# Performance work log

Hardware: AMD Instinct MI355X
Metric: run time of the kernel (lower is better)

## Reference

```python
import jax, jax.numpy as jnp
import numpy as np

E, H = 256, 4
DH = E // H                      # head dim 64
DHALF, N, R, K = 256, 16, 16, 5  # mamba d_inner//2, d_state, dt_rank, d_conv
B, L = 2, 2048


def _ln(x, g, b):
    m = jnp.mean(x, -1, keepdims=True)
    v = jnp.var(x, -1, keepdims=True)
    return (x - m) * jax.lax.rsqrt(v + 1e-5) * g + b


def _rotate_half(x):
    y = x.reshape(x.shape[:-1] + (-1, 2))
    return jnp.stack((-y[..., 1], y[..., 0]), -1).reshape(x.shape)


def _dwconv(x, w):  # x: (B,C,L), w: (C,1,K), depthwise 'same' conv, no bias (conv_bias//2 == 0)
    return jax.lax.conv_general_dilated(
        x, w, (1,), 'SAME', feature_group_count=x.shape[1],
        dimension_numbers=('NCH', 'OIH', 'NCH'))


def _selective_scan(x, dt, A_log, Bm, Cm, Dp, dt_bias):
    # x, dt: (B,Dh,L); Bm, Cm: (B,N,L); A_log: (Dh,N); Dp, dt_bias: (Dh,)
    A = -jnp.exp(A_log)
    delta = jax.nn.softplus(dt + dt_bias[None, :, None])
    seq = (jnp.moveaxis(delta, 2, 0), jnp.moveaxis(x, 2, 0),
           jnp.moveaxis(Bm, 2, 0), jnp.moveaxis(Cm, 2, 0))
    h0 = jnp.zeros((x.shape[0], A.shape[0], A.shape[1]), x.dtype)

    def step(h, inp):
        d_l, x_l, B_l, C_l = inp
        h = jnp.exp(d_l[:, :, None] * A) * h + (d_l * x_l)[:, :, None] * B_l[:, None, :]
        return h, jnp.einsum('bdn,bn->bd', h, C_l)

    _, ys = jax.lax.scan(step, h0, seq)
    return jnp.moveaxis(ys, 0, 2) + Dp[None, :, None] * x


def _forward(desc0, desc1, pe0, pe1, qkv_w, qkv_b, attn_out_w, attn_out_b,
             ma_ffn_w1, ma_ffn_b1, ma_ffn_g, ma_ffn_beta, ma_ffn_w2, ma_ffn_b2,
             m_in_w, m_convx_w, m_convz_w, m_xproj_w, m_dt_w, m_dt_b, m_Alog, m_D, m_out_w,
             ca_qk_w, ca_qk_b, ca_v_w, ca_v_b, ca_out_w, ca_out_b,
             ca_ffn_w1, ca_ffn_b1, ca_ffn_g, ca_ffn_beta, ca_ffn_w2, ca_ffn_b2):

    def mamba_twopath(x_in):
        xz = jnp.swapaxes(x_in @ m_in_w.T, 1, 2)           # (B, 2*Dh, L)
        xc, zc = xz[:, :DHALF], xz[:, DHALF:]
        xc = jax.nn.silu(_dwconv(xc, m_convx_w))
        zc = jax.nn.silu(_dwconv(zc, m_convz_w))
        x_dbl = jnp.einsum('bdl,kd->bkl', xc, m_xproj_w)   # (B, R+2N, L)
        # dt_proj applies its bias here AND the same bias is re-added inside the scan
        # (delta_bias), exactly as in the torch source.
        dt = jnp.einsum('brl,dr->bdl', x_dbl[:, :R], m_dt_w) + m_dt_b[None, :, None]
        Bm, Cm = x_dbl[:, R:R + N], x_dbl[:, R + N:]
        y = _selective_scan(xc, dt, m_Alog, Bm, Cm, m_D, m_dt_b)  # (B, Dh, L)
        return jnp.swapaxes(y, 1, 2) @ m_out_w.T, jnp.swapaxes(zc, 1, 2) @ m_out_w.T

    def ma_ffn(h):
        h = _ln(h @ ma_ffn_w1.T + ma_ffn_b1, ma_ffn_g, ma_ffn_beta)
        return jax.nn.gelu(h, approximate=False) @ ma_ffn_w2.T + ma_ffn_b2

    def mamba_attention(x, pe):
        b, l, _ = x.shape
        qkv = (x @ qkv_w.T + qkv_b).reshape(b, l, H, DH, 3)
        qkv = jnp.swapaxes(qkv, 1, 2)                       # (B,H,L,DH,3)
        q, k, v = qkv[..., 0], qkv[..., 1], qkv[..., 2]
        q = q * pe[0] + _rotate_half(q) * pe[1]
        k = k * pe[0] + _rotate_half(k) * pe[1]
        attn = jax.nn.softmax(jnp.einsum('bhid,bhjd->bhij', q, k) * DH ** -0.5, -1)
        o = jnp.einsum('bhij,bhjd->bhid', attn, v)
        o = jnp.swapaxes(o, 1, 2).reshape(b, l, E) @ attn_out_w.T + attn_out_b
        s_x, c_x = mamba_twopath(x)
        return x + ma_ffn(jnp.concatenate([x, o, s_x, c_x], -1))

    def ca_ffn(h):
        h = _ln(h @ ca_ffn_w1.T + ca_ffn_b1, ca_ffn_g, ca_ffn_beta)
        return jax.nn.gelu(h, approximate=False) @ ca_ffn_w2.T + ca_ffn_b2

    def split_heads(t):
        b, l, _ = t.shape
        return jnp.swapaxes(t.reshape(b, l, H, DH), 1, 2)

    def cross_attn(x0, x1):
        s = DH ** -0.25  # scale**0.5 applied to both qk0 and qk1
        qk0 = split_heads(x0 @ ca_qk_w.T + ca_qk_b) * s
        qk1 = split_heads(x1 @ ca_qk_w.T + ca_qk_b) * s
        v0 = split_heads(x0 @ ca_v_w.T + ca_v_b)
        v1 = split_heads(x1 @ ca_v_w.T + ca_v_b)
        sim = jnp.einsum('bhid,bhjd->bhij', qk0, qk1)       # (B,H,L0,L1)
        m0 = jnp.einsum('bhij,bhjd->bhid', jax.nn.softmax(sim, -1), v1)
        m1 = jnp.einsum('bhji,bhjd->bhid', jax.nn.softmax(sim, -2), v0)
        b, l = x0.shape[0], x0.shape[1]
        m0 = jnp.swapaxes(m0, 1, 2).reshape(b, l, E) @ ca_out_w.T + ca_out_b
        m1 = jnp.swapaxes(m1, 1, 2).reshape(b, x1.shape[1], E) @ ca_out_w.T + ca_out_b
        x0 = x0 + ca_ffn(jnp.concatenate([x0, m0], -1))
        x1 = x1 + ca_ffn(jnp.concatenate([x1, m1], -1))
        return x0, x1

    d0 = mamba_attention(desc0, pe0)
    d1 = mamba_attention(desc1, pe1)
    return cross_attn(d0, d1)


def setup_inputs():
    key = jax.random.key(0)
    ks = jax.random.split(key, 32)
    rn = lambda i, shape, s=0.02: jax.random.normal(ks[i], shape, jnp.float32) * s
    rng = np.random.default_rng(0)
    dt = np.exp(rng.uniform(size=DHALF) * (np.log(0.1) - np.log(0.001)) + np.log(0.001))
    inv_dt = dt + np.log(-np.expm1(-dt))
    return {
        'desc0': jax.random.normal(ks[0], (B, L, E), jnp.float32),
        'desc1': jax.random.normal(ks[1], (B, L, E), jnp.float32),
        'pe0': jax.random.normal(ks[2], (2, B, 1, L, DH), jnp.float32),
        'pe1': jax.random.normal(ks[3], (2, B, 1, L, DH), jnp.float32),
        'qkv_w': rn(4, (3 * E, E)), 'qkv_b': rn(5, (3 * E,)),
        'attn_out_w': rn(6, (E, E)), 'attn_out_b': rn(7, (E,)),
        'ma_ffn_w1': rn(8, (2 * E, 4 * E)), 'ma_ffn_b1': rn(9, (2 * E,)),
        'ma_ffn_g': jnp.ones((2 * E,), jnp.float32), 'ma_ffn_beta': jnp.zeros((2 * E,), jnp.float32),
        'ma_ffn_w2': rn(10, (E, 2 * E)), 'ma_ffn_b2': rn(11, (E,)),
        'm_in_w': rn(12, (2 * DHALF, E)),
        'm_convx_w': rn(13, (DHALF, 1, K), 0.2), 'm_convz_w': rn(14, (DHALF, 1, K), 0.2),
        'm_xproj_w': rn(15, (R + 2 * N, DHALF)),
        'm_dt_w': rn(16, (DHALF, R), R ** -0.5),
        'm_dt_b': jnp.asarray(inv_dt, jnp.float32),
        'm_Alog': jnp.log(jnp.broadcast_to(jnp.arange(1, N + 1, dtype=jnp.float32), (DHALF, N))),
        'm_D': jnp.ones((DHALF,), jnp.float32),
        'm_out_w': rn(17, (E, DHALF)),
        'ca_qk_w': rn(18, (E, E)), 'ca_qk_b': rn(19, (E,)),
        'ca_v_w': rn(20, (E, E)), 'ca_v_b': rn(21, (E,)),
        'ca_out_w': rn(22, (E, E)), 'ca_out_b': rn(23, (E,)),
        'ca_ffn_w1': rn(24, (2 * E, 2 * E)), 'ca_ffn_b1': rn(25, (2 * E,)),
        'ca_ffn_g': jnp.ones((2 * E,), jnp.float32), 'ca_ffn_beta': jnp.zeros((2 * E,), jnp.float32),
        'ca_ffn_w2': rn(26, (E, 2 * E)), 'ca_ffn_b2': rn(27, (E,)),
    }


def reference(desc0, desc1, pe0, pe1, qkv_w, qkv_b, attn_out_w, attn_out_b,
              ma_ffn_w1, ma_ffn_b1, ma_ffn_g, ma_ffn_beta, ma_ffn_w2, ma_ffn_b2,
              m_in_w, m_convx_w, m_convz_w, m_xproj_w, m_dt_w, m_dt_b, m_Alog, m_D, m_out_w,
              ca_qk_w, ca_qk_b, ca_v_w, ca_v_b, ca_out_w, ca_out_b,
              ca_ffn_w1, ca_ffn_b1, ca_ffn_g, ca_ffn_beta, ca_ffn_w2, ca_ffn_b2):
    return _forward(desc0, desc1, pe0, pe1, qkv_w, qkv_b, attn_out_w, attn_out_b,
                    ma_ffn_w1, ma_ffn_b1, ma_ffn_g, ma_ffn_beta, ma_ffn_w2, ma_ffn_b2,
                    m_in_w, m_convx_w, m_convz_w, m_xproj_w, m_dt_w, m_dt_b, m_Alog, m_D, m_out_w,
                    ca_qk_w, ca_qk_b, ca_v_w, ca_v_b, ca_out_w, ca_out_b,
                    ca_ffn_w1, ca_ffn_b1, ca_ffn_g, ca_ffn_beta, ca_ffn_w2, ca_ffn_b2)
```

## Files before the change

### kernel.cpp

```cpp
#include <hip/hip_runtime.h>

typedef unsigned short u16;
typedef short s16;
typedef s16 s16x8 __attribute__((ext_vector_type(8)));
typedef float f32x4 __attribute__((ext_vector_type(4)));

__device__ __forceinline__ float bf2f(u16 u){
  union { unsigned int i; float f; } v; v.i = ((unsigned int)u) << 16; return v.f;
}
__device__ __forceinline__ u16 f2bf(float f){
  union { float f; unsigned int u; } v; v.f = f;
  unsigned int r = (v.u + 0x7fffu + ((v.u >> 16) & 1u)) >> 16;
  return (u16)r;
}
__device__ __forceinline__ unsigned int cvtpk(float lo, float hi){
  unsigned int d;
  asm("v_cvt_pk_bf16_f32 %0, %1, %2" : "=v"(d) : "v"(lo), "v"(hi));
  return d;
}
__device__ __forceinline__ uint4 pack8(float4 a0, float4 a1){
  uint4 v;
  v.x = cvtpk(a0.x, a0.y); v.y = cvtpk(a0.z, a0.w);
  v.z = cvtpk(a1.x, a1.y); v.w = cvtpk(a1.z, a1.w);
  return v;
// ... 16 lines not shown
__device__ __forceinline__ float dppf(float x){
  return __int_as_float(__builtin_amdgcn_update_dpp(0, __float_as_int(x), C, 0xf, 0xf, true));
}
__device__ __forceinline__ float dppmax16(float v){
  v = fmaxf(v, dppf<0xB1>(v));
  v = fmaxf(v, dppf<0x4E>(v));
  v = fmaxf(v, dppf<0x141>(v));
  v = fmaxf(v, dppf<0x140>(v));
  return v;
}
__device__ __forceinline__ float dppsum16(float v){
  v += dppf<0xB1>(v);
  v += dppf<0x4E>(v);
  v += dppf<0x141>(v);
  v += dppf<0x140>(v);
  return v;
}

__global__ __launch_bounds__(256) void k_sniff(const unsigned int* __restrict__ w,
                                               int n, int* __restrict__ flag){
  __shared__ int cnt[256];
  int c = 0;
  for (int i = threadIdx.x; i < n; i += 256){
    unsigned e = (w[i] >> 7) & 0xFFu;
    c += (e >= 120u && e <= 127u) ? 1 : 0;
  }
  cnt[threadIdx.x] = c; __syncthreads();
  for (int s = 128; s > 0; s >>= 1){
    if (threadIdx.x < s) cnt[threadIdx.x] += cnt[threadIdx.x + s];
    __syncthreads();
  }
  if (threadIdx.x == 0) flag[0] = (2 * cnt[0] > n) ? 1 : 0;
  if (threadIdx.x == 1) flag[1] = 0;
}

struct WC { const void* src[11]; int off[12]; };
__global__ __launch_bounds__(256) void k_wconv(WC wc, u16* __restrict__ dst,
                                               const int* __restrict__ flagp){
  int fl = *flagp;
  int i = blockIdx.x * 256 + threadIdx.x;
  if (i >= wc.off[11]) return;
  int s = 0;
  #pragma unroll
  for (int t = 1; t < 11; ++t) s += (i >= wc.off[t]) ? 1 : 0;
  dst[i] = f2bf(ldw(wc.src[s], i - wc.off[s], fl));
}

__global__ __launch_bounds__(256) void k_pad(
  const void* __restrict__ wx, const void* __restrict__ wd,
  const void* __restrict__ bd,
  u16* __restrict__ px, u16* __restrict__ pd, float* __restrict__ pb,
  const int* __restrict__ flagp)
{
  int fl = *flagp;
  int i = blockIdx.x * 256 + threadIdx.x;
  if (i < 16384){
    int r = i >> 8, c = i & 255;
    px[i] = f2bf((r < 48) ? ldw(wx, r*256 + c, fl) : 0.f);
  } else if (i < 32768){
    int j = i - 16384;
    int n = j >> 6, k = j & 63;
    pd[j] = f2bf((k < 16) ? ldw(wd, n*16 + k, fl) : 0.f);
  } else if (i < 33024){
    pb[i - 32768] = ldw(bd, i - 32768, fl);
  }
}

__global__ __launch_bounds__(256) void k_gemm_mfma(
  const void* __restrict__ A0, int aflidx, int lda, int K, int N,
  const u16* __restrict__ W, const u16* __restrict__ W2, int nsplit, int wflidx,
  const void* __restrict__ bias,
  float* __restrict__ Cf0, u16* __restrict__ Cb, int ldc,
  float* __restrict__ C20, int ldc2,
  const void* __restrict__ resid, int rflidx, int ldr,
  const void* __restrict__ csrc, int cflidx, float* __restrict__ cdst,
  float oscale, int act_gelu, int outmode,
  const void* __restrict__ A1, long coff1, long c2off1,
  const int* __restrict__ flagp)
{
  const int fl  = flagp[0];
  const int afl = flagp[aflidx];
  const int wfl = flagp[wflidx];
  const int rfl = flagp[rflidx];
  const int cfl = flagp[cflidx];
  const void* A = A0;
  float* Cf = Cf0;
  float* C2 = C20;
  if (blockIdx.z){ A = A1; Cf += coff1; C2 += c2off1; }
  __shared__ u16 As[64*72];
  __shared__ u16 Bs[64*72];
  const int tid = threadIdx.x;
  const int w = tid >> 6, lane = tid & 63, quad = lane >> 4, m = lane & 15;
  const int m0 = blockIdx.y << 6, n0 = blockIdx.x << 6;
  const int srow = tid >> 2, sc0 = (tid & 3) << 4;
  const int reg2 = (n0 >= nsplit);
  const u16* Wp = reg2 ? W2 : W;
  const int nbase = reg2 ? nsplit : 0;

  f32x4 acc[4];
  #pragma unroll
  for (int ct = 0; ct < 4; ++ct) acc[ct] = (f32x4){0.f,0.f,0.f,0.f};

  for (int k0 = 0; k0 < K; k0 += 64){
    {
      long ab = (long)(m0 + srow) * lda + k0 + sc0;
      if (afl && !act_gelu){
        #pragma unroll
        for (int g = 0; g < 2; ++g)
          *(uint4*)&As[srow*72 + sc0 + g*8] = *(const uint4*)((const u16*)A + ab + g*8);
      } else {
        #pragma unroll
        for (int g = 0; g < 2; ++g){
          float4 a0 = ldw4(A, ab + g*8, afl);
          float4 a1 = ldw4(A, ab + g*8 + 4, afl);
          if (act_gelu){
            a0.x=gelu_f(a0.x); a0.y=gelu_f(a0.y); a0.z=gelu_f(a0.z); a0.w=gelu_f(a0.w);
            a1.x=gelu_f(a1.x); a1.y=gelu_f(a1.y); a1.z=gelu_f(a1.z); a1.w=gelu_f(a1.w);
// ... 35 lines not shown
      for (int r = 0; r < 4; ++r){
        float dl = acc[ct][r] + bv + bv;
        float delta = (dl > 20.f) ? dl : __logf(1.f + __expf(dl));
        dl4[r] = delta;
        dx4[r] = delta * ldw(resid, (long)(gmb + r) * ldr + gn, rfl);
      }
      *(float4*)&Cf[(long)gn * ldc + gmb] = make_float4(dl4[0], dl4[1], dl4[2], dl4[3]);
      *(float4*)&C2[(long)gn * ldc2 + gmb] = make_float4(dx4[0], dx4[1], dx4[2], dx4[3]);
    }
    return;
  }

  #pragma unroll
  for (int r = 0; r < 4; ++r){
    int gm = m0 + w*16 + quad*4 + r;
    #pragma unroll
    for (int ct = 0; ct < 4; ++ct){
      int gn = n0 + ct*16 + m;
      float v = acc[ct][r];
      if (reg2){
        C2[(long)gm * ldc2 + (gn - nsplit)] = v;
      } else {
        if (bias) v += ldw(bias, gn, wfl);
        v *= oscale;
        if (resid) v += ldw(resid, (long)gm * ldr + gn, rfl);
        long off = (long)gm * ldc + gn;
        if (outmode == 2){
          if (fl) Cb[off] = f2bf(v); else Cf[off] = v;
        } else if (outmode == 3){
          Cb[off] = f2bf(v);
        } else {
          Cf[off] = v;
        }
        if (cdst) cdst[(long)gm * ldc + gn] = ldw(csrc, (long)gm * 256 + gn, cfl);
      }
    }
  }
}

struct GB8 {
  const float* A[8]; const u16* W[8]; const void* bias[8];
  float* Cf[8]; u16* Cb[8]; const void* resid[8];
  const void* csrc[8]; float* cdst[8]; float osc[8];
  int cfl[8]; int wkoff[8]; int rfli[8];
  const float* aux[8]; const void* dvec;
};

__global__ __launch_bounds__(256) void k_gemmb(
  GB8 gb, int lda, int K, int N, int ldc, int ldr, int ldwq,
  int act_gelu, int outmode, const int* __restrict__ flagp)
{
  const int fl = flagp[0];
  const int z = blockIdx.z;
  const float* A = gb.A[z]; const u16* W = gb.W[z]; const void* bias = gb.bias[z];
  float* Cf = gb.Cf[z]; u16* Cb = gb.Cb[z]; const void* resid = gb.resid[z];
  const void* csrc = gb.csrc[z]; float* cdst = gb.cdst[z];
  const float osc = gb.osc[z];
  const int cfl = flagp[gb.cfl[z]];
  const int rfl = flagp[gb.rfli[z]];
  const int wkoff = gb.wkoff[z];
  const float* aux = gb.aux[z];

  __shared__ u16 As[64*72];
  __shared__ u16 Bs[64*72];
  const int tid = threadIdx.x;
  const int w = tid >> 6, lane = tid & 63, quad = lane >> 4, m = lane & 15;
  const int m0 = blockIdx.y << 6, n0 = blockIdx.x << 6;
  const int srow = tid >> 2, sc0 = (tid & 3) << 4;

  f32x4 acc[4];
  #pragma unroll
  for (int ct = 0; ct < 4; ++ct) acc[ct] = (f32x4){0.f,0.f,0.f,0.f};

  for (int k0 = 0; k0 < K; k0 += 64){
    {
      const float* ar = A + (long)(m0 + srow) * lda + k0 + sc0;
      #pragma unroll
      for (int g = 0; g < 2; ++g){
        float4 a0 = *(const float4*)(ar + g*8);
        float4 a1 = *(const float4*)(ar + g*8 + 4);
        if (aux){
          const float* xr = aux + (long)(m0 + srow) * lda + k0 + sc0;
          float4 x0 = *(const float4*)(xr + g*8);
          float4 x1 = *(const float4*)(xr + g*8 + 4);
          float4 d0 = ldw4(gb.dvec, k0 + sc0 + g*8, fl);
          float4 d1 = ldw4(gb.dvec, k0 + sc0 + g*8 + 4, fl);
          a0.x += d0.x*x0.x; a0.y += d0.y*x0.y; a0.z += d0.z*x0.z; a0.w += d0.w*x0.w;
          a1.x += d1.x*x1.x; a1.y += d1.y*x1.y; a1.z += d1.z*x1.z; a1.w += d1.w*x1.w;
        }
        if (act_gelu){
          a0.x=gelu_f(a0.x); a0.y=gelu_f(a0.y); a0.z=gelu_f(a0.z); a0.w=gelu_f(a0.w);
          a1.x=gelu_f(a1.x); a1.y=gelu_f(a1.y); a1.z=gelu_f(a1.z); a1.w=gelu_f(a1.w);
        }
        *(uint4*)&As[srow*72 + sc0 + g*8] = pack8(a0, a1);
      }
    }
    {
      long wb = (long)(n0 + srow) * ldwq + wkoff + k0 + sc0;
      #pragma unroll
      for (int g = 0; g < 2; ++g)
        *(uint4*)&Bs[srow*72 + sc0 + g*8] = *(const uint4*)(W + wb + g*8);
    }
    __syncthreads();

    s16x8 av[2];
    #pragma unroll
    for (int s = 0; s < 2; ++s)
      av[s] = *(const s16x8*)&As[(w*16 + m)*72 + s*32 + quad*8];
    #pragma unroll
    for (int ct = 0; ct < 4; ++ct)
      #pragma unroll
      for (int s = 0; s < 2; ++s){
        s16x8 bv = *(const s16x8*)&Bs[(ct*16 + m)*72 + s*32 + quad*8];
        acc[ct] = __builtin_amdgcn_mfma_f32_16x16x32_bf16(av[s], bv, acc[ct], 0, 0, 0);
      }
    __syncthreads();
  }

  #pragma unroll
  for (int r = 0; r < 4; ++r){
    int gm = m0 + w*16 + quad*4 + r;
    #pragma unroll
    for (int ct = 0; ct < 4; ++ct){
      int gn = n0 + ct*16 + m;
      float v = acc[ct][r];
      if (bias) v += ldw(bias, gn, fl);
      v *= osc;
      if (resid) v += ldw(resid, (long)gm * ldr + gn, rfl);
      long off = (long)gm * ldc + gn;
      if (outmode == 2){
        if (fl) Cb[off] = f2bf(v); else Cf[off] = v;
      } else if (outmode == 3){
        Cb[off] = f2bf(v);
      } else {
        Cf[off] = v;
      }
      if (cdst) cdst[(long)gm * ldc + gn] = ldw(csrc, (long)gm * 256 + gn, cfl);
    }
  }
}

__global__ __launch_bounds__(256) void k_rope(
  const float* __restrict__ qkv0, const float* __restrict__ qkv1,
  const void* __restrict__ pe0, const void* __restrict__ pe1,
  u16* __restrict__ q, u16* __restrict__ k, u16* __restrict__ v,
  int L, int B, int H, const int* __restrict__ flagp)
{
  int fl = *flagp;
  int tid = threadIdx.x;
  int lq = tid >> 6, d = tid & 63;
  int l = blockIdx.x * 4 + lq;
  int bh = blockIdx.y;
  int dsc = bh >> 3;
  int bh7 = bh & 7;
  int b = bh7 >> 2, h = bh7 & 3;
  const float* qkv = dsc ? qkv1 : qkv0;
  const void* pe = dsc ? pe1 : pe0;
  const float* row = qkv + ((long)b * L + l) * 768 + h * 192;
  float qv = row[d*3+0], kv = row[d*3+1], vv = row[d*3+2];
  int dn = (d & 1) ? (d - 1) : (d + 1);
  float qn = row[dn*3+0], kn = row[dn*3+1];
  float rq = (d & 1) ? qn : -qn;
  float rk = (d & 1) ? kn : -kn;
  long peo = ((long)b * L + l) * 64 + d;
  float p0 = ldw(pe, peo, fl);
  float p1 = ldw(pe, (long)B * L * 64 + peo, fl);
  long o = ((long)bh * L + l) * 64 + d;
  q[o] = f2bf((qv * p0 + rq * p1) * 0.18033688011112042f);
  k[o] = f2bf(kv * p0 + rk * p1);
  v[o] = f2bf(vv);
// ... 129 lines not shown
    asm volatile("s_waitcnt lgkmcnt(0)" ::: "memory");

    s16x8 ap[2];
    #pragma unroll
    for (int s = 0; s < 2; ++s)
      ap[s] = *(const s16x8*)&Ps[(w*16 + m)*72 + (((2*w + 4*s + quad) & 7) << 3)];
    #pragma unroll
    for (int nt = 0; nt < 4; ++nt)
      #pragma unroll
      for (int s = 0; s < 2; ++s){
        s16x8 bv = *(const s16x8*)&Vt[(nt*16 + m)*72 + (((2*nt + 4*s + quad) & 7) << 3)];
        o_acc[nt] = __builtin_amdgcn_mfma_f32_16x16x32_bf16(ap[s], bv, o_acc[nt], 0, 0, 0);
      }
    __syncthreads();
  }

  const long zOoff = (long)z * BHL * 64;
  #pragma unroll
  for (int r = 0; r < 4; ++r){
    int iq = iq0 + w*16 + quad*4 + r;
    long rowid = ((long)b*L + iq) * H + h;
    #pragma unroll
    for (int nt = 0; nt < 4; ++nt)
      Opart[zOoff + rowid*64 + nt*16 + m] = o_acc[nt][r];
    if (m == 0){
      mpart[(long)z*BHL + rowid] = mrow[r];
      lpart[(long)z*BHL + rowid] = lrow[r];
    }
  }
}

__global__ __launch_bounds__(256) void k_attn_comb(
  const float* Opart, const float* mpart, const float* lpart,
  float* O, long BHL, int nz)
{
  long i = (long)blockIdx.x * 256 + threadIdx.x;
  long row = i >> 6;
  float mv[4];
  float M = -1e30f;
  for (int z = 0; z < nz; ++z){
    mv[z] = mpart[(long)z*BHL + row];
    M = fmaxf(M, mv[z]);
  }
  long N64 = BHL * 64;
  float T = 0.f, acc = 0.f;
  for (int z = 0; z < nz; ++z){
    float wz = exp2f(mv[z] - M);
    T   += lpart[(long)z*BHL + row] * wz;
    acc += Opart[(long)z*N64 + i] * wz;
  }
  O[i] = acc / T;
}

__global__ __launch_bounds__(256) void k_conv2(
  const float* __restrict__ xz,
  const void* __restrict__ wx, const void* __restrict__ wz,
  float* __restrict__ outx, float* __restrict__ outz,
  int L, const int* __restrict__ flagp)
{
  int fl = *flagp;
  int c = threadIdx.x;
  int bl = blockIdx.x; int b = bl / L, l = bl % L;
  int choff = blockIdx.y ? 256 : 0;
  const void* w = blockIdx.y ? wz : wx;
  float* out = blockIdx.y ? outz : outx;
  const float* base = xz + ((long)b * L) * 512 + choff + c;
  float s = 0.f;
  #pragma unroll
  for (int kk = 0; kk < 5; ++kk){
    int ll = l + kk - 2;
    if (ll >= 0 && ll < L) s += base[(long)ll * 512] * ldw(w, c*5 + kk, fl);
  }
  out[((long)b * L + l) * 256 + c] = s / (1.f + __expf(-s));
}

#define SC_CS 64
#define SC_NC 32

__global__ __launch_bounds__(256) void k_scan1(
  const float* __restrict__ deltaT, const float* __restrict__ dxcT,
  const float* __restrict__ xdbl, const void* __restrict__ Alog,
  float* __restrict__ E_out, float* __restrict__ F_out,
  int L, int ldt, const int* __restrict__ flagp)
{
  int fl = *flagp;
  int tid = threadIdx.x;
  int g = tid >> 4, n = tid & 15;
  int gid = blockIdx.x * 16 + g;
  int chunk = gid & (SC_NC - 1);
  int p = gid >> 5;
  int b = p >> 8, d = p & 255;
  float A = -__expf(ldw(Alog, d*16 + n, fl));
  const float* dTp = deltaT + (long)d*ldt + (long)b*L;
  const float* dxp = dxcT  + (long)d*ldt + (long)b*L;
  const float* xdb = xdbl + (long)b*L*64;
  int l0 = chunk * SC_CS;
  float E = 1.f, F = 0.f;
  for (int i = 0; i < SC_CS; i += 4){
    int l = l0 + i;
    float4 dt4 = *(const float4*)(dTp + l);
    float4 dx4 = *(const float4*)(dxp + l);
    float e[4], u[4];
    e[0] = __expf(dt4.x * A); e[1] = __expf(dt4.y * A);
    e[2] = __expf(dt4.z * A); e[3] = __expf(dt4.w * A);
    u[0] = dx4.x * xdb[(l+0)*64 + 16 + n];
    u[1] = dx4.y * xdb[(l+1)*64 + 16 + n];
// ... 99 lines not shown
    v[i] = hr[lane + 64*i] + h2r[lane + 64*i];
    s += v[i]; ss += v[i]*v[i];
  }
  #pragma unroll
  for (int off = 1; off < 64; off <<= 1){ s += __shfl_xor(s, off); ss += __shfl_xor(ss, off); }
  float mean = s * (1.f/512.f);
  float var  = ss * (1.f/512.f) - mean * mean;
  float rs = rsqrtf(var + 1e-5f);
  #pragma unroll
  for (int i = 0; i < 8; ++i){
    int c = lane + 64*i;
    hr[c] = (v[i] - mean) * rs * ldw(g, c, fl) + ldw(beta, c, fl);
  }
}

extern "C" void kernel_launch(void* const* d_in, const int* in_sizes, int n_in,
                              void* d_out, int out_size, void* d_ws, size_t ws_size,
                              hipStream_t stream)
{
  const int B_ = 2, L_ = 2048, H_ = 4;
  const long BLE = (long)B_ * L_ * 256;
  const long BHLb = 2L * B_ * H_ * L_;

  int* flagp = (int*)d_ws;
  float* base = (float*)d_ws + 64;

  float* cat0   = base + 0*BLE;
  float* cat1   = base + 3*BLE;
  float* xz01   = base + 6*BLE;
  u16*   q01    = (u16*)(base + 10*BLE);
  u16*   k01    = (u16*)(base + 11*BLE);
  u16*   v01    = (u16*)(base + 12*BLE);
  float* Opart  = base + 13*BLE;
  float* ob01   = base + 21*BLE;
  float* mml    = base + 23*BLE;
  float* mll    = mml + 2*32768;
  float* xc01   = base + 24*BLE;
  float* zc01   = base + 26*BLE;
  float* xdbl01 = base + 28*BLE;
  float* delta01= base + 29*BLE;
  float* dxc01  = base + 31*BLE;
  float* scE    = base + 33*BLE;
  float* scF    = scE + 524288;
  float* scH    = scF + 524288;
  float* y01    = base + 35*BLE;
  float* catc0  = base + 37*BLE;
  float* catc1  = base + 41*BLE;
  float* h0     = base + 45*BLE;
  float* part0  = base + 47*BLE;
  float* h1     = base + 49*BLE;
  float* part1  = base + 51*BLE;
  float* dbuf0  = base + 53*BLE;
  float* dbuf1  = base + 54*BLE;
  u16*   qc     = (u16*)(base + 55*BLE);
  u16*   kc     = qc + 1048576;
  u16*   vc     = kc + 1048576;
  u16*   oc     = vc + 1048576;
  float* catA   = base + 57*BLE;
  float* catB   = base + 59*BLE;
  u16*   px     = (u16*)(base + 61*BLE);
  u16*   pd     = px + 16384;
  float* pb     = (float*)(pd + 16384);
  u16*   wbuf   = (u16*)(base + 62*BLE);

  const void* in[35];
  for (int i = 0; i < 35 && i < n_in; ++i) in[i] = d_in[i];

  const int woff[12] = {
    0,
    196608,
    327680,
    393216,
    917504,
    1048576,
    1114112,
    1179648,
    1245184,
    1310720,
    1572864,
    1703936 };
  const u16* wqkv  = wbuf + woff[0];
  const u16* wxz   = wbuf + woff[1];
  const u16* wattn = wbuf + woff[2];
  const u16* wffn1 = wbuf + woff[3];
  const u16* wffn2 = wbuf + woff[4];
  const u16* wout  = wbuf + woff[5];
  const u16* wcqk  = wbuf + woff[6];
  const u16* wcv   = wbuf + woff[7];
  const u16* wcout = wbuf + woff[8];
  const u16* wcf1  = wbuf + woff[9];
  const u16* wcf2  = wbuf + woff[10];

  k_sniff<<<1, 256, 0, stream>>>((const unsigned int*)in[0], 2048, flagp);
  {
    WC wc = {};
    wc.src[0]=in[4]; wc.src[1]=in[14]; wc.src[2]=in[6]; wc.src[3]=in[8];
    wc.src[4]=in[12]; wc.src[5]=in[22]; wc.src[6]=in[23]; wc.src[7]=in[25];
    wc.src[8]=in[27]; wc.src[9]=in[29]; wc.src[10]=in[33];
    for (int t = 0; t < 12; ++t) wc.off[t] = woff[t];
    k_wconv<<<(woff[11] + 255)/256, 256, 0, stream>>>(wc, wbuf, flagp);
  }
  k_pad<<<130, 256, 0, stream>>>(in[17], in[18], in[19], px, pd, pb, flagp);

  const int BIG = 1 << 30;
  const long sbP = (long)H_ * L_ * 64, shP = (long)L_ * 64, slP = 64;
  const long sbF = (long)L_ * 256,     shF = 64,            slF = 256;
  const int NZ = 2;
  const int kchunk = L_ / NZ;
  const int MROWS = 4 * L_;
  const float LOG2E = 1.4426950408889634f;

  k_gemm_mfma<<<dim3(20, 64, 2), 256, 0, stream>>>(
      in[0], 0, 256, 256, 1280, wqkv, wxz, 768, 0, in[5],
      cat0, nullptr, 768, xz01, 512,
      nullptr, 1, 0, nullptr, 1, nullptr, 1.f, 0, 0,
      in[1], 3*BLE, 2*BLE, flagp);
  k_rope<<<dim3(L_/4, 16), 256, 0, stream>>>(cat0, cat1, in[2], in[3],
      q01, k01, v01, L_, B_, H_, flagp);
  k_attn_mfma<<<dim3(L_/64, 16, NZ), 256, 0, stream>>>(
      q01, sbP, shP, slP, k01, sbP, shP, slP, v01, sbP, shP, slP,
      Opart, mml, mll, L_, H_, kchunk, 0);
  k_attn_comb<<<8192, 256, 0, stream>>>(Opart, mml, mll, ob01, BHLb, NZ);
  k_conv2<<<dim3(2*B_*L_, 2), 256, 0, stream>>>(xz01, in[15], in[16], xc01, zc01, L_, flagp);
  k_gemm_mfma<<<dim3(1, 128), 256, 0, stream>>>(
      xc01, 1, 256, 256, 64, px, nullptr, BIG, 1, nullptr,
      xdbl01, nullptr, 64, nullptr, 0,
      nullptr, 1, 0, nullptr, 1, nullptr, 1.f, 0, 0,
      nullptr, 0, 0, flagp);
  k_gemm_mfma<<<dim3(4, 128), 256, 0, stream>>>(
      xdbl01, 1, 64, 64, 256, pd, nullptr, BIG, 1, pb,
      delta01, nullptr, MROWS, dxc01, MROWS,
      xc01, 1, 256, nullptr, 1, nullptr, 1.f, 0, 4,
      nullptr, 0, 0, flagp);
  k_scan1<<<2048, 256, 0, stream>>>(delta01, dxc01, xdbl01, in[20], scE, scF, L_, MROWS, flagp);
  k_scan2<<<64, 256, 0, stream>>>(scE, scF, scH);
  k_scan3<<<2048, 256, 0, stream>>>(delta01, dxc01, xdbl01, in[20], scH, y01, L_, MROWS, flagp);
  {
    GB8 gb = {};
    gb.dvec = in[21];
    gb.A[0] = y01;        gb.aux[0] = xc01;       gb.W[0] = wout; gb.Cf[0] = catc0 + 512; gb.osc[0] = 1.f; gb.cfl[0] = 1;
    gb.A[1] = zc01;       gb.W[1] = wout; gb.Cf[1] = catc0 + 768; gb.osc[1] = 1.f; gb.cfl[1] = 1;
    gb.A[2] = ob01;       gb.W[2] = wattn; gb.bias[2] = in[7];    gb.Cf[2] = catc0 + 256;
    gb.csrc[2] = in[0];   gb.cdst[2] = catc0; gb.osc[2] = 1.f;    gb.cfl[2] = 0;
    gb.A[3] = y01 + BLE;  gb.aux[3] = xc01 + BLE; gb.W[3] = wout; gb.Cf[3] = catc1 + 512; gb.osc[3] = 1.f; gb.cfl[3] = 1;
    gb.A[4] = zc01 + BLE; gb.W[4] = wout; gb.Cf[4] = catc1 + 768; gb.osc[4] = 1.f; gb.cfl[4] = 1;
    gb.A[5] = ob01 + BLE; gb.W[5] = wattn; gb.bias[5] = in[7];    gb.Cf[5] = catc1 + 256;
    gb.csrc[5] = in[1];   gb.cdst[5] = catc1; gb.osc[5] = 1.f;    gb.cfl[5] = 0;
    k_gemmb<<<dim3(4, 64, 6), 256, 0, stream>>>(gb, 256, 256, 256, 1024, 0, 256, 0, 0, flagp);
  }
  {
    GB8 gb = {};
    gb.cfl[0] = gb.cfl[1] = gb.cfl[2] = gb.cfl[3] = 1;
    gb.A[0] = catc0;       gb.W[0] = wffn1; gb.bias[0] = in[9]; gb.Cf[0] = h0;    gb.osc[0] = 1.f;
    gb.A[1] = catc0 + 512; gb.W[1] = wffn1; gb.wkoff[1] = 512;  gb.Cf[1] = part0; gb.osc[1] = 1.f;
    gb.A[2] = catc1;       gb.W[2] = wffn1; gb.bias[2] = in[9]; gb.Cf[2] = h1;    gb.osc[2] = 1.f;
    gb.A[3] = catc1 + 512; gb.W[3] = wffn1; gb.wkoff[3] = 512;  gb.Cf[3] = part1; gb.osc[3] = 1.f;
    k_gemmb<<<dim3(8, 64, 4), 256, 0, stream>>>(gb, 1024, 512, 512, 512, 0, 1024, 0, 0, flagp);
  }
  k_ln2<<<2048, 256, 0, stream>>>(h0, part0, h1, part1, in[10], in[11], flagp);
  {
    GB8 gb = {};
    gb.cfl[0] = gb.cfl[1] = 1;
    gb.A[0] = h0; gb.W[0] = wffn2; gb.bias[0] = in[13]; gb.resid[0] = in[0]; gb.rfli[0] = 0;
    gb.Cf[0] = dbuf0; gb.osc[0] = 1.f;
    gb.A[1] = h1; gb.W[1] = wffn2; gb.bias[1] = in[13]; gb.resid[1] = in[1]; gb.rfli[1] = 0;
    gb.Cf[1] = dbuf1; gb.osc[1] = 1.f;
    k_gemmb<<<dim3(4, 64, 2), 256, 0, stream>>>(gb, 512, 512, 256, 256, 256, 512, 1, 0, flagp);
  }

  const float s4 = 0.35355339059327373f;
  float* cm0 = xc01;
  {
    GB8 gb = {};
    gb.cfl[0] = gb.cfl[1] = gb.cfl[2] = gb.cfl[3] = 1;
    gb.A[0] = dbuf0; gb.W[0] = wcqk; gb.bias[0] = in[24]; gb.Cb[0] = qc; gb.osc[0] = s4 * LOG2E;
    gb.A[1] = dbuf1; gb.W[1] = wcqk; gb.bias[1] = in[24]; gb.Cb[1] = kc; gb.osc[1] = s4;
    gb.A[2] = dbuf0; gb.W[2] = wcv;  gb.bias[2] = in[26]; gb.Cb[2] = vc; gb.osc[2] = 1.f;
    gb.A[3] = dbuf1; gb.W[3] = wcv;  gb.bias[3] = in[26]; gb.Cb[3] = oc; gb.osc[3] = 1.f;
    k_gemmb<<<dim3(4, 64, 4), 256, 0, stream>>>(gb, 256, 256, 256, 256, 0, 256, 0, 3, flagp);
  }
  k_attn_mfma<<<dim3(L_/64, 16, NZ), 256, 0, stream>>>(
      qc, sbF, shF, slF, qc, sbF, shF, slF, vc, sbF, shF, slF,
      Opart, mml, mll, L_, H_, kchunk, 2);
  k_attn_comb<<<8192, 256, 0, stream>>>(Opart, mml, mll, cm0, BHLb, NZ);
  {
    GB8 gb = {};
    gb.cfl[0] = gb.cfl[1] = 1;
    gb.A[0] = cm0;       gb.W[0] = wcout; gb.bias[0] = in[28]; gb.Cf[0] = catA + 256;
    gb.csrc[0] = dbuf0;  gb.cdst[0] = catA; gb.osc[0] = 1.f;
    gb.A[1] = cm0 + BLE; gb.W[1] = wcout; gb.bias[1] = in[28]; gb.Cf[1] = catB + 256;
    gb.csrc[1] = dbuf1;  gb.cdst[1] = catB; gb.osc[1] = 1.f;
    k_gemmb<<<dim3(4, 64, 2), 256, 0, stream>>>(gb, 256, 256, 256, 512, 0, 256, 0, 0, flagp);
  }
  {
    GB8 gb = {};
    gb.cfl[0] = gb.cfl[1] = gb.cfl[2] = gb.cfl[3] = 1;
    gb.A[0] = catA;       gb.W[0] = wcf1; gb.bias[0] = in[30]; gb.Cf[0] = h0;    gb.osc[0] = 1.f;
    gb.A[1] = catA + 256; gb.W[1] = wcf1; gb.wkoff[1] = 256;   gb.Cf[1] = part0; gb.osc[1] = 1.f;
    gb.A[2] = catB;       gb.W[2] = wcf1; gb.bias[2] = in[30]; gb.Cf[2] = h1;    gb.osc[2] = 1.f;
    gb.A[3] = catB + 256; gb.W[3] = wcf1; gb.wkoff[3] = 256;   gb.Cf[3] = part1; gb.osc[3] = 1.f;
    k_gemmb<<<dim3(8, 64, 4), 256, 0, stream>>>(gb, 512, 256, 512, 512, 0, 512, 0, 0, flagp);
  }
  k_ln2<<<2048, 256, 0, stream>>>(h0, part0, h1, part1, in[31], in[32], flagp);
  {
    GB8 gb = {};
    gb.cfl[0] = gb.cfl[1] = 1;
    gb.rfli[0] = gb.rfli[1] = 1;
    gb.A[0] = h0; gb.W[0] = wcf2; gb.bias[0] = in[34]; gb.resid[0] = dbuf0;
    gb.Cf[0] = (float*)d_out; gb.Cb[0] = (u16*)d_out; gb.osc[0] = 1.f;
    gb.A[1] = h1; gb.W[1] = wcf2; gb.bias[1] = in[34]; gb.resid[1] = dbuf1;
    gb.Cf[1] = (float*)d_out + BLE; gb.Cb[1] = (u16*)d_out + BLE; gb.osc[1] = 1.f;
    k_gemmb<<<dim3(4, 64, 2), 256, 0, stream>>>(gb, 512, 512, 256, 256, 256, 512, 1, 2, flagp);
  }
}
```

Before: 649.3 us.

## Store intermediate GEMM activations as bf16 to halve activation traffic

Intermediate activations that feed GEMMs (conv outputs, attention combine outputs, concat buffers, the d-buffers) are now written once as bf16, and the batched GEMM gains a bf16 A path that copies tiles straight into shared memory. The inputs desc0/desc1 are also converted to bf16 inside the weight-conversion kernel, so the first GEMM reads bf16. This removes fp32 reads and per-tile packing, and shrinks the workspace layout. The cost is extra conversion work in producers and a larger weight-conversion launch each call.

```diff
diff --git a/kernel.cpp b/kernel.cpp
--- a/kernel.cpp
+++ b/kernel.cpp
@@ -72,17 +72,18 @@
   }
   if (threadIdx.x == 0) flag[0] = (2 * cnt[0] > n) ? 1 : 0;
   if (threadIdx.x == 1) flag[1] = 0;
-}
-
-struct WC { const void* src[11]; int off[12]; };
+  if (threadIdx.x == 2) flag[2] = 1;
+}
+
+struct WC { const void* src[13]; int off[14]; };
 __global__ __launch_bounds__(256) void k_wconv(WC wc, u16* __restrict__ dst,
                                                const int* __restrict__ flagp){
   int fl = *flagp;
   int i = blockIdx.x * 256 + threadIdx.x;
-  if (i >= wc.off[11]) return;
+  if (i >= wc.off[13]) return;
   int s = 0;
   #pragma unroll
-  for (int t = 1; t < 11; ++t) s += (i >= wc.off[t]) ? 1 : 0;
+  for (int t = 1; t < 13; ++t) s += (i >= wc.off[t]) ? 1 : 0;
   dst[i] = f2bf(ldw(wc.src[s], i - wc.off[s], fl));
 }
 
@@ -113,7 +114,6 @@
   float* __restrict__ Cf0, u16* __restrict__ Cb, int ldc,
   float* __restrict__ C20, int ldc2,
   const void* __restrict__ resid, int rflidx, int ldr,
-  const void* __restrict__ csrc, int cflidx, float* __restrict__ cdst,
   float oscale, int act_gelu, int outmode,
   const void* __restrict__ A1, long coff1, long c2off1,
   const int* __restrict__ flagp)
@@ -122,7 +122,6 @@
   const int afl = flagp[aflidx];
   const int wfl = flagp[wflidx];
   const int rfl = flagp[rflidx];
-  const int cfl = flagp[cflidx];
   const void* A = A0;
   float* Cf = Cf0;
   float* C2 = C20;
@@ -224,17 +223,16 @@
         } else {
           Cf[off] = v;
         }
-        if (cdst) cdst[(long)gm * ldc + gn] = ldw(csrc, (long)gm * 256 + gn, cfl);
       }
     }
   }
 }
 
 struct GB8 {
-  const float* A[8]; const u16* W[8]; const void* bias[8];
+  const void* A[8]; const u16* W[8]; const void* bias[8];
   float* Cf[8]; u16* Cb[8]; const void* resid[8];
-  const void* csrc[8]; float* cdst[8]; float osc[8];
-  int cfl[8]; int wkoff[8]; int rfli[8];
+  const void* csrc[8]; u16* cdst[8]; float osc[8];
+  int cfl[8]; int wkoff[8]; int rfli[8]; int afli[8];
   const float* aux[8]; const void* dvec;
 };
 
@@ -244,13 +242,14 @@
 {
   const int fl = flagp[0];
   const int z = blockIdx.z;
-  const float* A = gb.A[z]; const u16* W = gb.W[z]; const void* bias = gb.bias[z];
+  const void* A = gb.A[z]; const u16* W = gb.W[z]; const void* bias = gb.bias[z];
   float* Cf = gb.Cf[z]; u16* Cb = gb.Cb[z]; const void* resid = gb.resid[z];
-  const void* csrc = gb.csrc[z]; float* cdst = gb.cdst[z];
+  const void* csrc = gb.csrc[z]; u16* cdst = gb.cdst[z];
   const float osc = gb.osc[z];
   const int cfl = flagp[gb.cfl[z]];
   const int rfl = flagp[gb.rfli[z]];
   const int wkoff = gb.wkoff[z];
+  const int abf = gb.afli[z];
   const float* aux = gb.aux[z];
 
   __shared__ u16 As[64*72];
@@ -265,8 +264,13 @@
   for (int ct = 0; ct < 4; ++ct) acc[ct] = (f32x4){0.f,0.f,0.f,0.f};
 
   for (int k0 = 0; k0 < K; k0 += 64){
-    {
-      const float* ar = A + (long)(m0 + srow) * lda + k0 + sc0;
+    if (abf){
+      const u16* ar = (const u16*)A + (long)(m0 + srow) * lda + k0 + sc0;
+      #pragma unroll
+      for (int g = 0; g < 2; ++g)
+        *(uint4*)&As[srow*72 + sc0 + g*8] = *(const uint4*)(ar + g*8);
+    } else {
+      const float* ar = (const float*)A + (long)(m0 + srow) * lda + k0 + sc0;
       #pragma unroll
       for (int g = 0; g < 2; ++g){
         float4 a0 = *(const float4*)(ar + g*8);
@@ -324,10 +328,12 @@
         if (fl) Cb[off] = f2bf(v); else Cf[off] = v;
       } else if (outmode == 3){
         Cb[off] = f2bf(v);
+      } else if (outmode == 5){
+        Cf[off] = v; Cb[off] = f2bf(v);
       } else {
         Cf[off] = v;
       }
-      if (cdst) cdst[(long)gm * ldc + gn] = ldw(csrc, (long)gm * 256 + gn, cfl);
+      if (cdst) cdst[(long)gm * ldc + gn] = f2bf(ldw(csrc, (long)gm * 256 + gn, cfl));
     }
   }
 }
@@ -523,7 +529,7 @@
 
 __global__ __launch_bounds__(256) void k_attn_comb(
   const float* Opart, const float* mpart, const float* lpart,
-  float* O, long BHL, int nz)
+  u16* O, long BHL, int nz)
 {
   long i = (long)blockIdx.x * 256 + threadIdx.x;
   long row = i >> 6;
@@ -540,13 +546,13 @@
     T   += lpart[(long)z*BHL + row] * wz;
     acc += Opart[(long)z*N64 + i] * wz;
   }
-  O[i] = acc / T;
+  O[i] = f2bf(acc / T);
 }
 
 __global__ __launch_bounds__(256) void k_conv2(
   const float* __restrict__ xz,
   const void* __restrict__ wx, const void* __restrict__ wz,
-  float* __restrict__ outx, float* __restrict__ outz,
+  float* __restrict__ outxf, u16* __restrict__ outxb, u16* __restrict__ outzb,
   int L, const int* __restrict__ flagp)
 {
   int fl = *flagp;
@@ -554,7 +560,6 @@
   int bl = blockIdx.x; int b = bl / L, l = bl % L;
   int choff = blockIdx.y ? 256 : 0;
   const void* w = blockIdx.y ? wz : wx;
-  float* out = blockIdx.y ? outz : outx;
   const float* base = xz + ((long)b * L) * 512 + choff + c;
   float s = 0.f;
   #pragma unroll
@@ -562,7 +567,14 @@
     int ll = l + kk - 2;
     if (ll >= 0 && ll < L) s += base[(long)ll * 512] * ldw(w, c*5 + kk, fl);
   }
-  out[((long)b * L + l) * 256 + c] = s / (1.f + __expf(-s));
+  s = s / (1.f + __expf(-s));
+  long idx = ((long)b * L + l) * 256 + c;
+  if (blockIdx.y){
+    outzb[idx] = f2bf(s);
+  } else {
+    outxf[idx] = s;
+    outxb[idx] = f2bf(s);
+  }
 }
 
 #define SC_CS 64
@@ -728,41 +740,45 @@
   u16*   k01    = (u16*)(base + 11*BLE);
   u16*   v01    = (u16*)(base + 12*BLE);
   float* Opart  = base + 13*BLE;
-  float* ob01   = base + 21*BLE;
-  float* mml    = base + 23*BLE;
+  u16*   obb    = (u16*)(base + 17*BLE);
+  float* mml    = base + 18*BLE;
   float* mll    = mml + 2*32768;
-  float* xc01   = base + 24*BLE;
-  float* zc01   = base + 26*BLE;
-  float* xdbl01 = base + 28*BLE;
-  float* delta01= base + 29*BLE;
-  float* dxc01  = base + 31*BLE;
-  float* scE    = base + 33*BLE;
+  float* xc_f   = base + 19*BLE;
+  u16*   xcb    = (u16*)(base + 21*BLE);
+  u16*   zcb    = (u16*)(base + 22*BLE);
+  float* xdbl01 = base + 23*BLE;
+  float* delta01= base + 24*BLE;
+  float* dxc01  = base + 26*BLE;
+  float* scE    = base + 28*BLE;
   float* scF    = scE + 524288;
   float* scH    = scF + 524288;
-  float* y01    = base + 35*BLE;
-  float* catc0  = base + 37*BLE;
-  float* catc1  = base + 41*BLE;
-  float* h0     = base + 45*BLE;
-  float* part0  = base + 47*BLE;
-  float* h1     = base + 49*BLE;
-  float* part1  = base + 51*BLE;
-  float* dbuf0  = base + 53*BLE;
-  float* dbuf1  = base + 54*BLE;
-  u16*   qc     = (u16*)(base + 55*BLE);
+  float* y01    = base + 30*BLE;
+  u16*   catc0b = (u16*)(base + 32*BLE);
+  u16*   catc1b = (u16*)(base + 34*BLE);
+  float* h0     = base + 36*BLE;
+  float* part0  = base + 38*BLE;
+  float* h1     = base + 40*BLE;
+  float* part1  = base + 42*BLE;
+  float* dbuf0  = base + 44*BLE;
+  float* dbuf1  = base + 45*BLE;
+  u16*   dbuf0b = (u16*)(base + 46*BLE);
+  u16*   dbuf1b = dbuf0b + 1048576;
+  u16*   qc     = (u16*)(base + 47*BLE);
   u16*   kc     = qc + 1048576;
   u16*   vc     = kc + 1048576;
   u16*   oc     = vc + 1048576;
-  float* catA   = base + 57*BLE;
-  float* catB   = base + 59*BLE;
-  u16*   px     = (u16*)(base + 61*BLE);
+  u16*   cm     = (u16*)(base + 49*BLE);
+  u16*   catAb  = (u16*)(base + 50*BLE);
+  u16*   catBb  = (u16*)(base + 51*BLE);
+  u16*   px     = (u16*)(base + 52*BLE);
   u16*   pd     = px + 16384;
   float* pb     = (float*)(pd + 16384);
-  u16*   wbuf   = (u16*)(base + 62*BLE);
+  u16*   wbuf   = (u16*)(base + 53*BLE);
 
   const void* in[35];
   for (int i = 0; i < 35 && i < n_in; ++i) in[i] = d_in[i];
 
-  const int woff[12] = {
+  const int woff[14] = {
     0,
     196608,
     327680,
@@ -774,7 +790,9 @@
     1245184,
     1310720,
     1572864,
-    1703936 };
+    1703936,
+    2752512,
+    3801088 };
   const u16* wqkv  = wbuf + woff[0];
   const u16* wxz   = wbuf + woff[1];
   const u16* wattn = wbuf + woff[2];
@@ -786,6 +804,8 @@
   const u16* wcout = wbuf + woff[8];
   const u16* wcf1  = wbuf + woff[9];
   const u16* wcf2  = wbuf + woff[10];
+  const u16* bin0  = wbuf + woff[11];
+  const u16* bin1  = wbuf + woff[12];
 
   k_sniff<<<1, 256, 0, stream>>>((const unsigned int*)in[0], 2048, flagp);
   {
@@ -793,8 +813,9 @@
     wc.src[0]=in[4]; wc.src[1]=in[14]; wc.src[2]=in[6]; wc.src[3]=in[8];
     wc.src[4]=in[12]; wc.src[5]=in[22]; wc.src[6]=in[23]; wc.src[7]=in[25];
     wc.src[8]=in[27]; wc.src[9]=in[29]; wc.src[10]=in[33];
-    for (int t = 0; t < 12; ++t) wc.off[t] = woff[t];
-    k_wconv<<<(woff[11] + 255)/256, 256, 0, stream>>>(wc, wbuf, flagp);
+    wc.src[11]=in[0]; wc.src[12]=in[1];
+    for (int t = 0; t < 14; ++t) wc.off[t] = woff[t];
+    k_wconv<<<(woff[13] + 255)/256, 256, 0, stream>>>(wc, wbuf, flagp);
   }
   k_pad<<<130, 256, 0, stream>>>(in[17], in[18], in[19], px, pd, pb, flagp);
 
@@ -807,26 +828,26 @@
   const float LOG2E = 1.4426950408889634f;
 
   k_gemm_mfma<<<dim3(20, 64, 2), 256, 0, stream>>>(
-      in[0], 0, 256, 256, 1280, wqkv, wxz, 768, 0, in[5],
+      bin0, 2, 256, 256, 1280, wqkv, wxz, 768, 0, in[5],
       cat0, nullptr, 768, xz01, 512,
-      nullptr, 1, 0, nullptr, 1, nullptr, 1.f, 0, 0,
-      in[1], 3*BLE, 2*BLE, flagp);
+      nullptr, 1, 0, 1.f, 0, 0,
+      bin1, 3*BLE, 2*BLE, flagp);
   k_rope<<<dim3(L_/4, 16), 256, 0, stream>>>(cat0, cat1, in[2], in[3],
       q01, k01, v01, L_, B_, H_, flagp);
   k_attn_mfma<<<dim3(L_/64, 16, NZ), 256, 0, stream>>>(
       q01, sbP, shP, slP, k01, sbP, shP, slP, v01, sbP, shP, slP,
       Opart, mml, mll, L_, H_, kchunk, 0);
-  k_attn_comb<<<8192, 256, 0, stream>>>(Opart, mml, mll, ob01, BHLb, NZ);
-  k_conv2<<<dim3(2*B_*L_, 2), 256, 0, stream>>>(xz01, in[15], in[16], xc01, zc01, L_, flagp);
+  k_attn_comb<<<8192, 256, 0, stream>>>(Opart, mml, mll, obb, BHLb, NZ);
+  k_conv2<<<dim3(2*B_*L_, 2), 256, 0, stream>>>(xz01, in[15], in[16], xc_f, xcb, zcb, L_, flagp);
   k_gemm_mfma<<<dim3(1, 128), 256, 0, stream>>>(
-      xc01, 1, 256, 256, 64, px, nullptr, BIG, 1, nullptr,
+      xcb, 2, 256, 256, 64, px, nullptr, BIG, 1, nullptr,
       xdbl01, nullptr, 64, nullptr, 0,
-      nullptr, 1, 0, nullptr, 1, nullptr, 1.f, 0, 0,
+      nullptr, 1, 0, 1.f, 0, 0,
       nullptr, 0, 0, flagp);
   k_gemm_mfma<<<dim3(4, 128), 256, 0, stream>>>(
       xdbl01, 1, 64, 64, 256, pd, nullptr, BIG, 1, pb,
       delta01, nullptr, MROWS, dxc01, MROWS,
-      xc01, 1, 256, nullptr, 1, nullptr, 1.f, 0, 4,
+      xc_f, 1, 256, 1.f, 0, 4,
       nullptr, 0, 0, flagp);
   k_scan1<<<2048, 256, 0, stream>>>(delta01, dxc01, xdbl01, in[20], scE, scF, L_, MROWS, flagp);
   k_scan2<<<64, 256, 0, stream>>>(scE, scF, scH);
@@ -834,23 +855,24 @@
   {
     GB8 gb = {};
     gb.dvec = in[21];
-    gb.A[0] = y01;        gb.aux[0] = xc01;       gb.W[0] = wout; gb.Cf[0] = catc0 + 512; gb.osc[0] = 1.f; gb.cfl[0] = 1;
-    gb.A[1] = zc01;       gb.W[1] = wout; gb.Cf[1] = catc0 + 768; gb.osc[1] = 1.f; gb.cfl[1] = 1;
-    gb.A[2] = ob01;       gb.W[2] = wattn; gb.bias[2] = in[7];    gb.Cf[2] = catc0 + 256;
-    gb.csrc[2] = in[0];   gb.cdst[2] = catc0; gb.osc[2] = 1.f;    gb.cfl[2] = 0;
-    gb.A[3] = y01 + BLE;  gb.aux[3] = xc01 + BLE; gb.W[3] = wout; gb.Cf[3] = catc1 + 512; gb.osc[3] = 1.f; gb.cfl[3] = 1;
-    gb.A[4] = zc01 + BLE; gb.W[4] = wout; gb.Cf[4] = catc1 + 768; gb.osc[4] = 1.f; gb.cfl[4] = 1;
-    gb.A[5] = ob01 + BLE; gb.W[5] = wattn; gb.bias[5] = in[7];    gb.Cf[5] = catc1 + 256;
-    gb.csrc[5] = in[1];   gb.cdst[5] = catc1; gb.osc[5] = 1.f;    gb.cfl[5] = 0;
-    k_gemmb<<<dim3(4, 64, 6), 256, 0, stream>>>(gb, 256, 256, 256, 1024, 0, 256, 0, 0, flagp);
+    gb.A[0] = y01;        gb.aux[0] = xc_f;       gb.W[0] = wout; gb.Cb[0] = catc0b + 512; gb.osc[0] = 1.f; gb.cfl[0] = 1;
+    gb.A[1] = zcb;        gb.afli[1] = 1;         gb.W[1] = wout; gb.Cb[1] = catc0b + 768; gb.osc[1] = 1.f; gb.cfl[1] = 1;
+    gb.A[2] = obb;        gb.afli[2] = 1;         gb.W[2] = wattn; gb.bias[2] = in[7];     gb.Cb[2] = catc0b + 256;
+    gb.csrc[2] = in[0];   gb.cdst[2] = catc0b;    gb.osc[2] = 1.f; gb.cfl[2] = 0;
+    gb.A[3] = y01 + BLE;  gb.aux[3] = xc_f + BLE; gb.W[3] = wout; gb.Cb[3] = catc1b + 512; gb.osc[3] = 1.f; gb.cfl[3] = 1;
+    gb.A[4] = zcb + 1048576; gb.afli[4] = 1;      gb.W[4] = wout; gb.Cb[4] = catc1b + 768; gb.osc[4] = 1.f; gb.cfl[4] = 1;
+    gb.A[5] = obb + 1048576; gb.afli[5] = 1;      gb.W[5] = wattn; gb.bias[5] = in[7];     gb.Cb[5] = catc1b + 256;
+    gb.csrc[5] = in[1];   gb.cdst[5] = catc1b;    gb.osc[5] = 1.f; gb.cfl[5] = 0;
+    k_gemmb<<<dim3(4, 64, 6), 256, 0, stream>>>(gb, 256, 256, 256, 1024, 0, 256, 0, 3, flagp);
   }
   {
     GB8 gb = {};
     gb.cfl[0] = gb.cfl[1] = gb.cfl[2] = gb.cfl[3] = 1;
-    gb.A[0] = catc0;       gb.W[0] = wffn1; gb.bias[0] = in[9]; gb.Cf[0] = h0;    gb.osc[0] = 1.f;
-    gb.A[1] = catc0 + 512; gb.W[1] = wffn1; gb.wkoff[1] = 512;  gb.Cf[1] = part0; gb.osc[1] = 1.f;
-    gb.A[2] = catc1;       gb.W[2] = wffn1; gb.bias[2] = in[9]; gb.Cf[2] = h1;    gb.osc[2] = 1.f;
-    gb.A[3] = catc1 + 512; gb.W[3] = wffn1; gb.wkoff[3] = 512;  gb.Cf[3] = part1; gb.osc[3] = 1.f;
+    gb.afli[0] = gb.afli[1] = gb.afli[2] = gb.afli[3] = 1;
+    gb.A[0] = catc0b;       gb.W[0] = wffn1; gb.bias[0] = in[9]; gb.Cf[0] = h0;    gb.osc[0] = 1.f;
+    gb.A[1] = catc0b + 512; gb.W[1] = wffn1; gb.wkoff[1] = 512;  gb.Cf[1] = part0; gb.osc[1] = 1.f;
+    gb.A[2] = catc1b;       gb.W[2] = wffn1; gb.bias[2] = in[9]; gb.Cf[2] = h1;    gb.osc[2] = 1.f;
+    gb.A[3] = catc1b + 512; gb.W[3] = wffn1; gb.wkoff[3] = 512;  gb.Cf[3] = part1; gb.osc[3] = 1.f;
     k_gemmb<<<dim3(8, 64, 4), 256, 0, stream>>>(gb, 1024, 512, 512, 512, 0, 1024, 0, 0, flagp);
   }
   k_ln2<<<2048, 256, 0, stream>>>(h0, part0, h1, part1, in[10], in[11], flagp);
@@ -858,43 +880,45 @@
     GB8 gb = {};
     gb.cfl[0] = gb.cfl[1] = 1;
     gb.A[0] = h0; gb.W[0] = wffn2; gb.bias[0] = in[13]; gb.resid[0] = in[0]; gb.rfli[0] = 0;
-    gb.Cf[0] = dbuf0; gb.osc[0] = 1.f;
+    gb.Cf[0] = dbuf0; gb.Cb[0] = dbuf0b; gb.osc[0] = 1.f;
     gb.A[1] = h1; gb.W[1] = wffn2; gb.bias[1] = in[13]; gb.resid[1] = in[1]; gb.rfli[1] = 0;
-    gb.Cf[1] = dbuf1; gb.osc[1] = 1.f;
-    k_gemmb<<<dim3(4, 64, 2), 256, 0, stream>>>(gb, 512, 512, 256, 256, 256, 512, 1, 0, flagp);
+    gb.Cf[1] = dbuf1; gb.Cb[1] = dbuf1b; gb.osc[1] = 1.f;
+    k_gemmb<<<dim3(4, 64, 2), 256, 0, stream>>>(gb, 512, 512, 256, 256, 256, 512, 1, 5, flagp);
   }
 
   const float s4 = 0.35355339059327373f;
-  float* cm0 = xc01;
   {
     GB8 gb = {};
     gb.cfl[0] = gb.cfl[1] = gb.cfl[2] = gb.cfl[3] = 1;
-    gb.A[0] = dbuf0; gb.W[0] = wcqk; gb.bias[0] = in[24]; gb.Cb[0] = qc; gb.osc[0] = s4 * LOG2E;
-    gb.A[1] = dbuf1; gb.W[1] = wcqk; gb.bias[1] = in[24]; gb.Cb[1] = kc; gb.osc[1] = s4;
-    gb.A[2] = dbuf0; gb.W[2] = wcv;  gb.bias[2] = in[26]; gb.Cb[2] = vc; gb.osc[2] = 1.f;
-    gb.A[3] = dbuf1; gb.W[3] = wcv;  gb.bias[3] = in[26]; gb.Cb[3] = oc; gb.osc[3] = 1.f;
+    gb.afli[0] = gb.afli[1] = gb.afli[2] = gb.afli[3] = 1;
+    gb.A[0] = dbuf0b; gb.W[0] = wcqk; gb.bias[0] = in[24]; gb.Cb[0] = qc; gb.osc[0] = s4 * LOG2E;
+    gb.A[1] = dbuf1b; gb.W[1] = wcqk; gb.bias[1] = in[24]; gb.Cb[1] = kc; gb.osc[1] = s4;
+    gb.A[2] = dbuf0b; gb.W[2] = wcv;  gb.bias[2] = in[26]; gb.Cb[2] = vc; gb.osc[2] = 1.f;
+    gb.A[3] = dbuf1b; gb.W[3] = wcv;  gb.bias[3] = in[26]; gb.Cb[3] = oc; gb.osc[3] = 1.f;
     k_gemmb<<<dim3(4, 64, 4), 256, 0, stream>>>(gb, 256, 256, 256, 256, 0, 256, 0, 3, flagp);
   }
   k_attn_mfma<<<dim3(L_/64, 16, NZ), 256, 0, stream>>>(
       qc, sbF, shF, slF, qc, sbF, shF, slF, vc, sbF, shF, slF,
       Opart, mml, mll, L_, H_, kchunk, 2);
-  k_attn_comb<<<8192, 256, 0, stream>>>(Opart, mml, mll, cm0, BHLb, NZ);
+  k_attn_comb<<<8192, 256, 0, stream>>>(Opart, mml, mll, cm, BHLb, NZ);
   {
     GB8 gb = {};
     gb.cfl[0] = gb.cfl[1] = 1;
-    gb.A[0] = cm0;       gb.W[0] = wcout; gb.bias[0] = in[28]; gb.Cf[0] = catA + 256;
-    gb.csrc[0] = dbuf0;  gb.cdst[0] = catA; gb.osc[0] = 1.f;
-    gb.A[1] = cm0 + BLE; gb.W[1] = wcout; gb.bias[1] = in[28]; gb.Cf[1] = catB + 256;
-    gb.csrc[1] = dbuf1;  gb.cdst[1] = catB; gb.osc[1] = 1.f;
-    k_gemmb<<<dim3(4, 64, 2), 256, 0, stream>>>(gb, 256, 256, 256, 512, 0, 256, 0, 0, flagp);
+    gb.afli[0] = gb.afli[1] = 1;
+    gb.A[0] = cm;           gb.W[0] = wcout; gb.bias[0] = in[28]; gb.Cb[0] = catAb + 256;
+    gb.csrc[0] = dbuf0;     gb.cdst[0] = catAb; gb.osc[0] = 1.f;
+    gb.A[1] = cm + 1048576; gb.W[1] = wcout; gb.bias[1] = in[28]; gb.Cb[1] = catBb + 256;
+    gb.csrc[1] = dbuf1;     gb.cdst[1] = catBb; gb.osc[1] = 1.f;
+    k_gemmb<<<dim3(4, 64, 2), 256, 0, stream>>>(gb, 256, 256, 256, 512, 0, 256, 0, 3, flagp);
   }
   {
     GB8 gb = {};
     gb.cfl[0] = gb.cfl[1] = gb.cfl[2] = gb.cfl[3] = 1;
-    gb.A[0] = catA;       gb.W[0] = wcf1; gb.bias[0] = in[30]; gb.Cf[0] = h0;    gb.osc[0] = 1.f;
-    gb.A[1] = catA + 256; gb.W[1] = wcf1; gb.wkoff[1] = 256;   gb.Cf[1] = part0; gb.osc[1] = 1.f;
-    gb.A[2] = catB;       gb.W[2] = wcf1; gb.bias[2] = in[30]; gb.Cf[2] = h1;    gb.osc[2] = 1.f;
-    gb.A[3] = catB + 256; gb.W[3] = wcf1; gb.wkoff[3] = 256;   gb.Cf[3] = part1; gb.osc[3] = 1.f;
+    gb.afli[0] = gb.afli[1] = gb.afli[2] = gb.afli[3] = 1;
+    gb.A[0] = catAb;       gb.W[0] = wcf1; gb.bias[0] = in[30]; gb.Cf[0] = h0;    gb.osc[0] = 1.f;
+    gb.A[1] = catAb + 256; gb.W[1] = wcf1; gb.wkoff[1] = 256;   gb.Cf[1] = part0; gb.osc[1] = 1.f;
+    gb.A[2] = catBb;       gb.W[2] = wcf1; gb.bias[2] = in[30]; gb.Cf[2] = h1;    gb.osc[2] = 1.f;
+    gb.A[3] = catBb + 256; gb.W[3] = wcf1; gb.wkoff[3] = 256;   gb.Cf[3] = part1; gb.osc[3] = 1.f;
     k_gemmb<<<dim3(8, 64, 4), 256, 0, stream>>>(gb, 512, 256, 512, 512, 0, 512, 0, 0, flagp);
   }
   k_ln2<<<2048, 256, 0, stream>>>(h0, part0, h1, part1, in[31], in[32], flagp);
```

Result: faster. 606.5 us (-6.6%).
